# Kernel optimization log

Measured on AMD Instinct MI355X. Metric: run time of the kernel, lower is better.

## Reference

```python
import jax, jax.numpy as jnp
import numpy as np

EMBED_DIM = 2048
NUM_HEADS = 16
HEAD_DIM = EMBED_DIM // NUM_HEADS
SCALE = 1.0 / float(np.sqrt(HEAD_DIM))
B, L = 2, 2048


def setup_inputs() -> dict:
    key = jax.random.key(0)
    ks = jax.random.split(key, 8)
    s_in = 1.0 / np.sqrt(EMBED_DIM)
    return {
        "query": jax.random.normal(ks[0], (B, L, EMBED_DIM), dtype=jnp.float32),
        "key": jax.random.normal(ks[1], (B, L, EMBED_DIM), dtype=jnp.float32),
        "value": jax.random.normal(ks[2], (B, L, EMBED_DIM), dtype=jnp.float32),
        # in_proj: Linear(E, 3E) -> weight [3E, E], bias [3E]
        "W_in": jax.random.uniform(ks[3], (3 * EMBED_DIM, EMBED_DIM), jnp.float32, -s_in, s_in),
        "b_in": jax.random.uniform(ks[4], (3 * EMBED_DIM,), jnp.float32, -s_in, s_in),
        # out_proj: Linear(E, E) -> weight [E, E], bias [E]
        "W_out": jax.random.uniform(ks[5], (EMBED_DIM, EMBED_DIM), jnp.float32, -s_in, s_in),
        "b_out": jax.random.uniform(ks[6], (EMBED_DIM,), jnp.float32, -s_in, s_in),
    }


def reference(query, key, value, W_in, b_in, W_out, b_out):
    # NOTE: the torch module ignores `key`/`value`; QKV all come from `query`.
    b, t, e = query.shape
    qkv = jnp.einsum("ble,fe->blf", query, W_in) + b_in  # [B, L, 3E]
    q, k, v = jnp.split(qkv, 3, axis=-1)
    # [B, H, L, D]
    q = q.reshape(b, t, NUM_HEADS, HEAD_DIM).transpose(0, 2, 1, 3)
    k = k.reshape(b, -1, NUM_HEADS, HEAD_DIM).transpose(0, 2, 1, 3)
    v = v.reshape(b, -1, NUM_HEADS, HEAD_DIM).transpose(0, 2, 1, 3)
    scores = jnp.einsum("bhqd,bhkd->bhqk", q, k) * SCALE  # [B, H, L, L]
    attn = jax.nn.softmax(scores, axis=-1)
    # torch code zeros attn if any NaN appears (can't happen with no masks);
    # replicate the guard harmlessly:
    attn = jnp.where(jnp.any(jnp.isnan(attn)), jnp.zeros_like(attn), attn)
    ctx = jnp.einsum("bhqk,bhkd->bhqd", attn, v)  # [B, H, L, D]
    ctx = ctx.transpose(0, 2, 1, 3).reshape(b, t, e)  # [B, L, E]
    out = jnp.einsum("ble,fe->blf", ctx, W_out) + b_out
    attn_avg = attn.mean(axis=1)  # [B, L, L]
    return (out, attn_avg)
```

## Files before the change

### kernel.cpp

```cpp
#include <hip/hip_runtime.h>
#include <hip/hip_bf16.h>
#include <stdint.h>
#include <stddef.h>

constexpr int BATCH = 2;
constexpr int SEQ   = 2048;
constexpr int EMBD  = 2048;
constexpr int NHEAD = 16;
constexpr int HDIM  = 128;
constexpr float QSCALE = 0.08838834764831845f * 1.4426950408889634f;

typedef short bf16x8 __attribute__((ext_vector_type(8)));
typedef float f32x4  __attribute__((ext_vector_type(4)));

__device__ __forceinline__ short f2bfs(float f) {
  union { __hip_bfloat16 h; short s; } u;
  u.h = __float2bfloat16(f);
  return u.s;
}

__device__ __forceinline__ void gload_lds16(const void* g, void* l) {
  __builtin_amdgcn_global_load_lds(
      (const __attribute__((address_space(1))) unsigned int*)g,
      (__attribute__((address_space(3))) unsigned int*)l, 16, 0, 0);
}

__device__ __forceinline__ int vperm(int k) {
  return (k & ~31) | (k & 3) | (((k >> 4) & 1) << 2) | (((k >> 2) & 3) << 3);
}

__global__ void cvt_bf16(const float* __restrict__ in, unsigned short* __restrict__ out, int n) {
  int i = (blockIdx.x * blockDim.x + threadIdx.x) * 8;
  const int stride = gridDim.x * blockDim.x * 8;
  for (; i + 7 < n; i += stride) {
    float4 a = *(const float4*)(in + i);
    float4 b = *(const float4*)(in + i + 4);
    union { unsigned short u[8]; int4 v; } r;
    r.u[0] = (unsigned short)f2bfs(a.x); r.u[1] = (unsigned short)f2bfs(a.y);
    r.u[2] = (unsigned short)f2bfs(a.z); r.u[3] = (unsigned short)f2bfs(a.w);
    r.u[4] = (unsigned short)f2bfs(b.x); r.u[5] = (unsigned short)f2bfs(b.y);
    r.u[6] = (unsigned short)f2bfs(b.z); r.u[7] = (unsigned short)f2bfs(b.w);
    *(int4*)(out + i) = r.v;
  }
}

struct EpiQKV {
  const float* bias;
  unsigned short* qs; unsigned short* ks; unsigned short* vti;
  __device__ void operator()(int row, int col, float v) const {
    float val = v + bias[col];
    const int which = col >> 11;
    const int h = (col >> 7) & 15;
    const int d = col & 127;
    const int b = row >> 11, l = row & (SEQ - 1);
    if (which == 0) {
      qs[(((unsigned)(b * NHEAD + h) * SEQ) + l) * HDIM + d] = (unsigned short)f2bfs(val * QSCALE);
    } else if (which == 1) {
      ks[(((unsigned)(b * NHEAD + h) * SEQ) + l) * HDIM + d] = (unsigned short)f2bfs(val);
    } else {
      vti[(((unsigned)(b * NHEAD + h) * HDIM) + d) * SEQ + vperm(l)] = (unsigned short)f2bfs(val);
    }
  }
};

struct EpiOut {
  const float* bias;
  float* out;
  __device__ void operator()(int row, int col, float v) const {
    out[(size_t)row * EMBD + col] = v + bias[col];
  }
};

template <class Epi>
__global__ __launch_bounds__(256, 2) void gemm_bt(
    const unsigned short* __restrict__ A, const unsigned short* __restrict__ B,
    int K, Epi epi) {
  __shared__ __align__(16) unsigned short lds[2][8192];
  const int tid = threadIdx.x;
  const int w = tid >> 6, lane = tid & 63;
  const int g = lane >> 4, lr = lane & 15;
  const int wm = w >> 1, wn = w & 1;
  const int m0 = blockIdx.y * 128, n0 = blockIdx.x * 128;
  const int srow = lane >> 2, sslot = lane & 3;

  f32x4 acc[4][4] = {};

  auto stage = [&](int buf, int t) {
    const int k0 = t * 32;
#pragma unroll
    for (int c2 = 0; c2 < 2; ++c2) {
      const int chunk = 2 * w + c2;
      const int row = chunk * 16 + srow;
      const int kel = k0 + ((sslot ^ ((row >> 1) & 3)) << 3);
      gload_lds16(A + (size_t)(m0 + row) * K + kel, &lds[buf][chunk * 512]);
      gload_lds16(B + (size_t)(n0 + row) * K + kel, &lds[buf][4096 + chunk * 512]);
    }
  };

  const int nt = K >> 5;
  int cur = 0;
  stage(0, 0);
  asm volatile("s_waitcnt vmcnt(0)" ::: "memory");
  __syncthreads();

  for (int t = 0; t < nt; ++t) {
    if (t + 1 < nt) stage(cur ^ 1, t + 1);
    bf16x8 af[4], bq[4];
#pragma unroll
    for (int fr = 0; fr < 4; ++fr) {
      const int r = wm * 64 + fr * 16 + lr;
      af[fr] = *(const bf16x8*)&lds[cur][r * 32 + ((g ^ ((r >> 1) & 3)) << 3)];
      const int rn = wn * 64 + fr * 16 + lr;
      bq[fr] = *(const bf16x8*)&lds[cur][4096 + rn * 32 + ((g ^ ((rn >> 1) & 3)) << 3)];
    }
#pragma unroll
    for (int i = 0; i < 4; ++i)
#pragma unroll
      for (int j = 0; j < 4; ++j)
        acc[i][j] = __builtin_amdgcn_mfma_f32_16x16x32_bf16(af[i], bq[j], acc[i][j], 0, 0, 0);
    asm volatile("s_waitcnt vmcnt(0)" ::: "memory");
    __syncthreads();
    cur ^= 1;
  }

#pragma unroll
  for (int i = 0; i < 4; ++i)
#pragma unroll
    for (int j = 0; j < 4; ++j) {
      const int row = m0 + wm * 64 + i * 16 + g * 4;
      const int col = n0 + wn * 64 + j * 16 + lr;
#pragma unroll
      for (int jr = 0; jr < 4; ++jr) epi(row + jr, col, acc[i][j][jr]);
    }
}

__global__ __launch_bounds__(256, 2) void flash_fwd(
    const unsigned short* __restrict__ qs, const unsigned short* __restrict__ ks,
    const unsigned short* __restrict__ vti, unsigned short* __restrict__ ctx,
    float* __restrict__ c_s) {
  __shared__ __align__(16) unsigned short smem[2][16384];
  const int tid = threadIdx.x, w = tid >> 6, lane = tid & 63;
  const int g = lane >> 4, lr = lane & 15;
  const int blk = blockIdx.x;
  const int qt = blk & 31, h = (blk >> 5) & 15, b = blk >> 9;
  const int q0 = qt * 64;
  const size_t bh = ((size_t)(b * NHEAD + h)) * SEQ * HDIM;

  const int qrow = q0 + w * 16 + lr;
  bf16x8 qf[4];
#pragma unroll
  for (int kk = 0; kk < 4; ++kk)
    qf[kk] = *(const bf16x8*)(qs + bh + (size_t)qrow * HDIM + kk * 32 + g * 8);

  float m_run = -1e30f, l_run = 0.f;
  f32x4 o[8] = {};

  auto stage = [&](int buf, int t) {
    unsigned short* kt = smem[buf];
    unsigned short* vt = smem[buf] + 8192;
    const int key0 = t * 64;
#pragma unroll
    for (int c = 0; c < 4; ++c) {
      const int chunk = w * 4 + c;
      const int key = chunk * 4 + (lane >> 4);
      const int slot = lane & 15;
      gload_lds16(ks + bh + (size_t)(key0 + key) * HDIM + ((slot ^ (key & 7)) * 8),
                  &kt[chunk * 512]);
    }
#pragma unroll
    for (int c = 0; c < 4; ++c) {
      const int chunk = w * 4 + c;
      const int d = chunk * 8 + (lane >> 3);
      const int slot = lane & 7;
      gload_lds16(vti + bh + (size_t)d * SEQ + key0 + ((slot ^ (d & 7)) * 8),
                  &vt[chunk * 512]);
    }
  };

  stage(0, 0);
  asm volatile("s_waitcnt vmcnt(0)" ::: "memory");
  __syncthreads();
  int cur = 0;

  for (int t = 0; t < 32; ++t) {
    if (t + 1 < 32) stage(cur ^ 1, t + 1);
    const unsigned short* kt = smem[cur];
    const unsigned short* vt = smem[cur] + 8192;

    f32x4 st[4] = {};
#pragma unroll
    for (int kk = 0; kk < 4; ++kk)
#pragma unroll
      for (int fc = 0; fc < 4; ++fc) {
        const int key = fc * 16 + lr;
        bf16x8 kf = *(const bf16x8*)&kt[key * 128 + (((kk * 4 + g) ^ (key & 7)) << 3)];
        st[fc] = __builtin_amdgcn_mfma_f32_16x16x32_bf16(kf, qf[kk], st[fc], 0, 0, 0);
      }

    float tmax = st[0][0];
#pragma unroll
    for (int fc = 0; fc < 4; ++fc)
#pragma unroll
      for (int j = 0; j < 4; ++j) tmax = fmaxf(tmax, st[fc][j]);
    tmax = fmaxf(tmax, __shfl_xor(tmax, 16));
    tmax = fmaxf(tmax, __shfl_xor(tmax, 32));
    if (!__all(tmax <= m_run + 8.f)) {
      const float m_new = fmaxf(m_run, tmax);
      const float corr = __builtin_exp2f(m_run - m_new);
      l_run *= corr;
#pragma unroll
      for (int fd = 0; fd < 8; ++fd)
#pragma unroll
        for (int j = 0; j < 4; ++j) o[fd][j] *= corr;
      m_run = m_new;
    }
    float pt[4][4];
    float tsum = 0.f;
#pragma unroll
    for (int fc = 0; fc < 4; ++fc)
#pragma unroll
      for (int j = 0; j < 4; ++j) {
        const float e = __builtin_exp2f(st[fc][j] - m_run);
        pt[fc][j] = e; tsum += e;
      }
    tsum += __shfl_xor(tsum, 16);
    tsum += __shfl_xor(tsum, 32);
    l_run += tsum;

    bf16x8 pb[2];
#pragma unroll
    for (int c = 0; c < 2; ++c)
#pragma unroll
      for (int j = 0; j < 4; ++j) {
        pb[c][j]     = f2bfs(pt[2 * c][j]);
        pb[c][4 + j] = f2bfs(pt[2 * c + 1][j]);
      }

#pragma unroll
    for (int fd = 0; fd < 8; ++fd) {
      const int d = fd * 16 + lr;
#pragma unroll
      for (int c = 0; c < 2; ++c) {
        bf16x8 vf = *(const bf16x8*)&vt[d * 64 + (((c * 4 + g) ^ (d & 7)) << 3)];
        o[fd] = __builtin_amdgcn_mfma_f32_16x16x32_bf16(vf, pb[c], o[fd], 0, 0, 0);
      }
    }

    asm volatile("s_waitcnt vmcnt(0)" ::: "memory");
    __syncthreads();
    cur ^= 1;
  }

  const float inv_l = 1.0f / l_run;
  unsigned short* trp = smem[0] + w * 2176;
#pragma unroll
  for (int fd = 0; fd < 8; ++fd)
#pragma unroll
    for (int jp = 0; jp < 2; ++jp) {
      const int d = fd * 16 + 4 * g + 2 * jp;
      unsigned valu = (unsigned)(unsigned short)f2bfs(o[fd][2 * jp] * inv_l) |
                      ((unsigned)(unsigned short)f2bfs(o[fd][2 * jp + 1] * inv_l) << 16);
      *(unsigned*)((char*)trp + lr * 272 + d * 2) = valu;
    }
  __syncthreads();
#pragma unroll
  for (int r4 = 0; r4 < 4; ++r4) {
    const int row = r4 * 4 + g;
    bf16x8 valv = *(const bf16x8*)((char*)trp + row * 272 + lr * 16);
    *(bf16x8*)(ctx + (size_t)(b * SEQ + q0 + w * 16 + row) * EMBD + h * HDIM + lr * 8) = valv;
  }
  if (g == 0) {
    const int ridx = (b * NHEAD + h) * SEQ + q0 + w * 16 + lr;
    c_s[ridx] = m_run + __log2f(l_run) + 4.0f;
  }
}

__global__ __launch_bounds__(256, 2) void attn_avg_k(
    const unsigned short* __restrict__ qs, const unsigned short* __restrict__ ks,
    const float* __restrict__ c_s, float* __restrict__ out) {
  __shared__ __align__(16) unsigned short lds[32768];
  unsigned short* qlds = lds;
  unsigned short* klds = lds + 16384;
  const int tid = threadIdx.x, w = tid >> 6, lane = tid & 63;
  const int g = lane >> 4, lr = lane & 15;
  const int wm = w >> 1, wn = w & 1;
  const int blk = blockIdx.x;
  const int k0 = (blk & 15) * 128, q0 = ((blk >> 4) & 15) * 128, b = blk >> 8;

  const int srow = lane >> 4, sslot = lane & 15;

  f32x4 acc[4][4] = {};

  for (int h = 0; h < NHEAD; ++h) {
    const size_t bh = ((size_t)(b * NHEAD + h)) * SEQ * HDIM;
    if (h) __syncthreads();
#pragma unroll
    for (int c = 0; c < 8; ++c) {
      const int chunk = w * 8 + c;
      const int row = chunk * 4 + srow;
      const int kel = (sslot ^ (row & 15)) * 8;
      gload_lds16(qs + bh + (size_t)(q0 + row) * HDIM + kel, &qlds[chunk * 512]);
      gload_lds16(ks + bh + (size_t)(k0 + row) * HDIM + kel, &klds[chunk * 512]);
    }
    asm volatile("s_waitcnt vmcnt(0)" ::: "memory");
    __syncthreads();

    f32x4 st[4][4] = {};
#pragma unroll
    for (int kk = 0; kk < 4; ++kk) {
      bf16x8 af[4], bq[4];
#pragma unroll
      for (int fr = 0; fr < 4; ++fr) {
        const int rq = wm * 64 + fr * 16 + lr;
        af[fr] = *(const bf16x8*)&qlds[rq * 128 + (((kk * 4 + g) ^ (rq & 15)) << 3)];
        const int rk = wn * 64 + fr * 16 + lr;
        bq[fr] = *(const bf16x8*)&klds[rk * 128 + (((kk * 4 + g) ^ (rk & 15)) << 3)];
      }
#pragma unroll
      for (int i = 0; i < 4; ++i)
#pragma unroll
        for (int j = 0; j < 4; ++j)
          st[i][j] = __builtin_amdgcn_mfma_f32_16x16x32_bf16(af[i], bq[j], st[i][j], 0, 0, 0);
    }

    const int chq = (b * NHEAD + h) * SEQ + q0 + wm * 64 + g * 4;
#pragma unroll
    for (int i = 0; i < 4; ++i) {
      const f32x4 cq = *(const f32x4*)&c_s[chq + i * 16];
#pragma unroll
      for (int j = 0; j < 4; ++j)
#pragma unroll
        for (int jr = 0; jr < 4; ++jr)
          acc[i][j][jr] += __builtin_exp2f(st[i][j][jr] - cq[jr]);
    }
  }

#pragma unroll
  for (int i = 0; i < 4; ++i)
#pragma unroll
    for (int jr = 0; jr < 4; ++jr) {
      const size_t rowoff = (size_t)(b * SEQ + q0 + wm * 64 + i * 16 + g * 4 + jr) * SEQ;
#pragma unroll
      for (int j = 0; j < 4; ++j)
        out[rowoff + k0 + wn * 64 + j * 16 + lr] = acc[i][j][jr];
    }
}

extern "C" void kernel_launch(void* const* d_in, const int* in_sizes, int n_in,
                              void* d_out, int out_size, void* d_ws, size_t ws_size,
                              hipStream_t stream) {
  const float* query = (const float*)d_in[0];
  const float* W_in  = (const float*)d_in[3];
  const float* b_in  = (const float*)d_in[4];
  const float* W_out = (const float*)d_in[5];
  const float* b_out = (const float*)d_in[6];

  float* out      = (float*)d_out;
  float* attn_avg = out + (size_t)BATCH * SEQ * EMBD;

  char* ws = (char*)d_ws;
  auto take = [&](size_t bytes) { char* p = ws; ws += bytes; return p; };
  const size_t szBLE = (size_t)BATCH * SEQ * EMBD * 2;
  unsigned short* qbf = (unsigned short*)take(szBLE);
  unsigned short* wi  = (unsigned short*)take((size_t)3 * EMBD * EMBD * 2);
  unsigned short* wo  = (unsigned short*)take((size_t)EMBD * EMBD * 2);
  unsigned short* qsb = (unsigned short*)take(szBLE);
  unsigned short* ksb = (unsigned short*)take(szBLE);
  unsigned short* vti = (unsigned short*)take(szBLE);
  unsigned short* ctx = (unsigned short*)take(szBLE);
  float* c_s = (float*)take((size_t)BATCH * NHEAD * SEQ * 4);

  cvt_bf16<<<1024, 256, 0, stream>>>(query, qbf, BATCH * SEQ * EMBD);
  cvt_bf16<<<2048, 256, 0, stream>>>(W_in, wi, 3 * EMBD * EMBD);
  cvt_bf16<<<1024, 256, 0, stream>>>(W_out, wo, EMBD * EMBD);

  gemm_bt<EpiQKV><<<dim3(48, 32), 256, 0, stream>>>(qbf, wi, EMBD,
                                                    EpiQKV{b_in, qsb, ksb, vti});
  flash_fwd<<<BATCH * NHEAD * (SEQ / 64), 256, 0, stream>>>(qsb, ksb, vti, ctx, c_s);
  gemm_bt<EpiOut><<<dim3(16, 32), 256, 0, stream>>>(ctx, wo, EMBD, EpiOut{b_out, out});
  attn_avg_k<<<BATCH * (SEQ / 128) * (SEQ / 128), 256, 0, stream>>>(qsb, ksb, c_s, attn_avg);
}
```

Before: 411.4 us.

## Use 256x256-tile 8-wave pipelined GEMM for QKV projection

Adds a new GEMM kernel with 256x256 output tiles, 512 threads and a 64-wide K step, used for the QKV input projection. It splits each K step into four quadrant phases that interleave LDS reads, next-tile global-to-LDS loads and MFMA bursts under s_setprio. It also remaps block IDs across 8 groups, likely to match the XCD layout and improve L2 reuse. The larger tile cuts global and LDS traffic per FLOP, at the cost of more registers and 128KB of LDS per block. The fixed-count vmcnt waits and the barrier-heavy schedule are fragile if any load count changes.

```diff
diff --git a/kernel.cpp b/kernel.cpp
--- a/kernel.cpp
+++ b/kernel.cpp
@@ -72,6 +72,135 @@
 };
 
 template <class Epi>
+__global__ __launch_bounds__(512, 2) void gemm_bt8(
+    const unsigned short* __restrict__ A, const unsigned short* __restrict__ B,
+    const int K, const int NBX, Epi epi) {
+  __shared__ __align__(16) unsigned short lds[2][32768];
+  const int tid = threadIdx.x, w = tid >> 6, lane = tid & 63;
+  const int g = lane >> 4, lr = lane & 15;
+  const int wm = w >> 2, wn = w & 3;
+
+  const int cpx = gridDim.x >> 3;
+  const int bid = ((int)blockIdx.x & 7) * cpx + ((int)blockIdx.x >> 3);
+  const int m0 = (bid / NBX) * 256, n0 = (bid % NBX) * 256;
+
+  const int nt = K >> 6;
+  const int srow = tid >> 3, sslot = tid & 7;
+
+  auto stageA = [&](int t, int hh) {
+    const int kel = t * 64 + ((sslot ^ (srow & 7)) << 3);
+#pragma unroll
+    for (int l = 0; l < 2; ++l)
+      gload_lds16(A + (size_t)(m0 + hh * 128 + l * 64 + srow) * K + kel,
+                  &lds[t & 1][hh * 8192 + l * 4096 + w * 512]);
+  };
+  auto stageB = [&](int t, int hh) {
+    const int kel = t * 64 + ((sslot ^ (srow & 7)) << 3);
+#pragma unroll
+    for (int l = 0; l < 2; ++l)
+      gload_lds16(B + (size_t)(n0 + hh * 128 + l * 64 + srow) * K + kel,
+                  &lds[t & 1][16384 + hh * 8192 + l * 4096 + w * 512]);
+  };
+  auto rdA = [&](int buf, int Mh, int kk, int fr) -> bf16x8 {
+    const int row = wm * 128 + Mh * 64 + fr * 16 + lr;
+    return *(const bf16x8*)&lds[buf][row * 64 + (((kk * 4 + g) ^ (row & 7)) << 3)];
+  };
+  auto rdB = [&](int buf, int Nh, int kk, int fb) -> bf16x8 {
+    const int row = wn * 64 + Nh * 32 + fb * 16 + lr;
+    return *(const bf16x8*)&lds[buf][16384 + row * 64 + (((kk * 4 + g) ^ (row & 7)) << 3)];
+  };
+
+  f32x4 acc[8][4] = {};
+  bf16x8 a[4][2], bn0[2][2], bn1[2][2];
+
+  stageA(0, 0); stageA(0, 1); stageB(0, 0); stageB(0, 1);
+  if (nt > 1) { stageA(1, 0);
+    asm volatile("s_waitcnt vmcnt(2)" ::: "memory");
+  } else {
+    asm volatile("s_waitcnt vmcnt(0)" ::: "memory");
+  }
+  __builtin_amdgcn_s_barrier();
+
+  for (int t = 0; t < nt; ++t) {
+    const int buf = t & 1;
+#pragma unroll
+    for (int fr = 0; fr < 4; ++fr) { a[fr][0] = rdA(buf, 0, 0, fr); a[fr][1] = rdA(buf, 0, 1, fr); }
+#pragma unroll
+    for (int fb = 0; fb < 2; ++fb) { bn0[fb][0] = rdB(buf, 0, 0, fb); bn0[fb][1] = rdB(buf, 0, 1, fb); }
+    if (t + 1 < nt) stageA(t + 1, 1);
+    __builtin_amdgcn_s_barrier();
+    asm volatile("s_waitcnt lgkmcnt(0)" ::: "memory");
+    __builtin_amdgcn_s_setprio(1);
+#pragma unroll
+    for (int fr = 0; fr < 4; ++fr)
+#pragma unroll
+      for (int fb = 0; fb < 2; ++fb)
+#pragma unroll
+        for (int kk = 0; kk < 2; ++kk)
+          acc[fr][fb] = __builtin_amdgcn_mfma_f32_16x16x32_bf16(a[fr][kk], bn0[fb][kk], acc[fr][fb], 0, 0, 0);
+    __builtin_amdgcn_s_setprio(0);
+    __builtin_amdgcn_s_barrier();
+#pragma unroll
+    for (int fb = 0; fb < 2; ++fb) { bn1[fb][0] = rdB(buf, 1, 0, fb); bn1[fb][1] = rdB(buf, 1, 1, fb); }
+    if (t + 1 < nt) stageB(t + 1, 0);
+    __builtin_amdgcn_s_barrier();
+    asm volatile("s_waitcnt lgkmcnt(0)" ::: "memory");
+    __builtin_amdgcn_s_setprio(1);
+#pragma unroll
+    for (int fr = 0; fr < 4; ++fr)
+#pragma unroll
+      for (int fb = 0; fb < 2; ++fb)
+#pragma unroll
+        for (int kk = 0; kk < 2; ++kk)
+          acc[fr][2 + fb] = __builtin_amdgcn_mfma_f32_16x16x32_bf16(a[fr][kk], bn1[fb][kk], acc[fr][2 + fb], 0, 0, 0);
+    __builtin_amdgcn_s_setprio(0);
+    __builtin_amdgcn_s_barrier();
+#pragma unroll
+    for (int fr = 0; fr < 4; ++fr) { a[fr][0] = rdA(buf, 1, 0, fr); a[fr][1] = rdA(buf, 1, 1, fr); }
+    if (t + 1 < nt) stageB(t + 1, 1);
+    __builtin_amdgcn_s_barrier();
+    asm volatile("s_waitcnt lgkmcnt(0)" ::: "memory");
+    __builtin_amdgcn_s_setprio(1);
+#pragma unroll
+    for (int fr = 0; fr < 4; ++fr)
+#pragma unroll
+      for (int fb = 0; fb < 2; ++fb)
+#pragma unroll
+        for (int kk = 0; kk < 2; ++kk)
+          acc[4 + fr][2 + fb] = __builtin_amdgcn_mfma_f32_16x16x32_bf16(a[fr][kk], bn1[fb][kk], acc[4 + fr][2 + fb], 0, 0, 0);
+    __builtin_amdgcn_s_setprio(0);
+    __builtin_amdgcn_s_barrier();
+    if (t + 2 < nt) stageA(t + 2, 0);
+    __builtin_amdgcn_s_barrier();
+    __builtin_amdgcn_s_setprio(1);
+#pragma unroll
+    for (int fr = 0; fr < 4; ++fr)
+#pragma unroll
+      for (int fb = 0; fb < 2; ++fb)
+#pragma unroll
+        for (int kk = 0; kk < 2; ++kk)
+          acc[4 + fr][fb] = __builtin_amdgcn_mfma_f32_16x16x32_bf16(a[fr][kk], bn0[fb][kk], acc[4 + fr][fb], 0, 0, 0);
+    __builtin_amdgcn_s_setprio(0);
+    if (t + 2 < nt) {
+      asm volatile("s_waitcnt vmcnt(2)" ::: "memory");
+    } else if (t + 1 < nt) {
+      asm volatile("s_waitcnt vmcnt(0)" ::: "memory");
+    }
+    __builtin_amdgcn_s_barrier();
+  }
+
+#pragma unroll
+  for (int mf = 0; mf < 8; ++mf)
+#pragma unroll
+    for (int nf = 0; nf < 4; ++nf) {
+      const int row = m0 + wm * 128 + mf * 16 + g * 4;
+      const int col = n0 + wn * 64 + nf * 16 + lr;
+#pragma unroll
+      for (int jr = 0; jr < 4; ++jr) epi(row + jr, col, acc[mf][nf][jr]);
+    }
+}
+
+template <class Epi>
 __global__ __launch_bounds__(256, 2) void gemm_bt(
     const unsigned short* __restrict__ A, const unsigned short* __restrict__ B,
     int K, Epi epi) {
@@ -374,8 +503,8 @@
   cvt_bf16<<<2048, 256, 0, stream>>>(W_in, wi, 3 * EMBD * EMBD);
   cvt_bf16<<<1024, 256, 0, stream>>>(W_out, wo, EMBD * EMBD);
 
-  gemm_bt<EpiQKV><<<dim3(48, 32), 256, 0, stream>>>(qbf, wi, EMBD,
-                                                    EpiQKV{b_in, qsb, ksb, vti});
+  gemm_bt8<EpiQKV><<<384, 512, 0, stream>>>(qbf, wi, EMBD, 24,
+                                            EpiQKV{b_in, qsb, ksb, vti});
   flash_fwd<<<BATCH * NHEAD * (SEQ / 64), 256, 0, stream>>>(qsb, ksb, vti, ctx, c_s);
   gemm_bt<EpiOut><<<dim3(16, 32), 256, 0, stream>>>(ctx, wo, EMBD, EpiOut{b_out, out});
   attn_avg_k<<<BATCH * (SEQ / 128) * (SEQ / 128), 256, 0, stream>>>(qsb, ksb, c_s, attn_avg);
```

Result: no change. 419.3 us (+1.9%).

## Triple-buffer Q/K staging in attn_avg kernel with per-32-dim chunk pipelining

Applied to the files above, without the earlier changes.

Replaces the per-head load-all-then-compute scheme in the attention-average kernel with a 3-slot ring buffer of 32-dim chunks of Q and K, prefetching two chunks ahead. Waits now use vmcnt(4) plus raw s_barrier instead of a full drain each head, so global loads can overlap MFMA work. LDS use drops from 64KB to 48KB per block, and the swizzle changes to match 32-element rows. The price is more barriers per head and some risk of subtle ring-buffer synchronisation mistakes.

```diff
diff --git a/kernel.cpp b/kernel.cpp
--- a/kernel.cpp
+++ b/kernel.cpp
@@ -278,52 +278,64 @@
 __global__ __launch_bounds__(256, 2) void attn_avg_k(
     const unsigned short* __restrict__ qs, const unsigned short* __restrict__ ks,
     const float* __restrict__ c_s, float* __restrict__ out) {
-  __shared__ __align__(16) unsigned short lds[32768];
-  unsigned short* qlds = lds;
-  unsigned short* klds = lds + 16384;
+  __shared__ __align__(16) unsigned short lds[3][8192];
   const int tid = threadIdx.x, w = tid >> 6, lane = tid & 63;
   const int g = lane >> 4, lr = lane & 15;
   const int wm = w >> 1, wn = w & 1;
   const int blk = blockIdx.x;
   const int k0 = (blk & 15) * 128, q0 = ((blk >> 4) & 15) * 128, b = blk >> 8;
-
-  const int srow = lane >> 4, sslot = lane & 15;
+  const int srow = lane >> 2, sslot = lane & 3;
+
+  constexpr int NC = NHEAD * 4;
+
+  auto stage = [&](int c) {
+    const size_t bh = ((size_t)(b * NHEAD + (c >> 2))) * SEQ * HDIM + (c & 3) * 32;
+    unsigned short* slot = lds[c % 3];
+#pragma unroll
+    for (int c2 = 0; c2 < 2; ++c2) {
+      const int chunk = 2 * w + c2;
+      const int row = chunk * 16 + srow;
+      const int kel = (sslot ^ ((row >> 1) & 3)) << 3;
+      gload_lds16(qs + bh + (size_t)(q0 + row) * HDIM + kel, &slot[chunk * 512]);
+      gload_lds16(ks + bh + (size_t)(k0 + row) * HDIM + kel, &slot[4096 + chunk * 512]);
+    }
+  };
 
   f32x4 acc[4][4] = {};
 
-  for (int h = 0; h < NHEAD; ++h) {
-    const size_t bh = ((size_t)(b * NHEAD + h)) * SEQ * HDIM;
-    if (h) __syncthreads();
-#pragma unroll
-    for (int c = 0; c < 8; ++c) {
-      const int chunk = w * 8 + c;
-      const int row = chunk * 4 + srow;
-      const int kel = (sslot ^ (row & 15)) * 8;
-      gload_lds16(qs + bh + (size_t)(q0 + row) * HDIM + kel, &qlds[chunk * 512]);
-      gload_lds16(ks + bh + (size_t)(k0 + row) * HDIM + kel, &klds[chunk * 512]);
-    }
-    asm volatile("s_waitcnt vmcnt(0)" ::: "memory");
-    __syncthreads();
-
+  stage(0); stage(1);
+  asm volatile("s_waitcnt vmcnt(4)" ::: "memory");
+  asm volatile("s_barrier" ::: "memory");
+
+  for (int hc = 0; hc < NHEAD; ++hc) {
     f32x4 st[4][4] = {};
 #pragma unroll
-    for (int kk = 0; kk < 4; ++kk) {
+    for (int dq = 0; dq < 4; ++dq) {
+      const int c = hc * 4 + dq;
+      if (c + 2 < NC) stage(c + 2);
+      const unsigned short* slot = lds[c % 3];
       bf16x8 af[4], bq[4];
 #pragma unroll
       for (int fr = 0; fr < 4; ++fr) {
         const int rq = wm * 64 + fr * 16 + lr;
-        af[fr] = *(const bf16x8*)&qlds[rq * 128 + (((kk * 4 + g) ^ (rq & 15)) << 3)];
+        af[fr] = *(const bf16x8*)&slot[rq * 32 + ((g ^ ((rq >> 1) & 3)) << 3)];
         const int rk = wn * 64 + fr * 16 + lr;
-        bq[fr] = *(const bf16x8*)&klds[rk * 128 + (((kk * 4 + g) ^ (rk & 15)) << 3)];
+        bq[fr] = *(const bf16x8*)&slot[4096 + rk * 32 + ((g ^ ((rk >> 1) & 3)) << 3)];
       }
 #pragma unroll
       for (int i = 0; i < 4; ++i)
 #pragma unroll
         for (int j = 0; j < 4; ++j)
           st[i][j] = __builtin_amdgcn_mfma_f32_16x16x32_bf16(af[i], bq[j], st[i][j], 0, 0, 0);
-    }
-
-    const int chq = (b * NHEAD + h) * SEQ + q0 + wm * 64 + g * 4;
+      if (c + 2 < NC) {
+        asm volatile("s_waitcnt vmcnt(4)" ::: "memory");
+        asm volatile("s_barrier" ::: "memory");
+      } else if (c + 1 < NC) {
+        asm volatile("s_waitcnt vmcnt(0)" ::: "memory");
+        asm volatile("s_barrier" ::: "memory");
+      }
+    }
+    const int chq = (b * NHEAD + hc) * SEQ + q0 + wm * 64 + g * 4;
 #pragma unroll
     for (int i = 0; i < 4; ++i) {
       const f32x4 cq = *(const f32x4*)&c_s[chq + i * 16];
```

Result: faster. 399.0 us (-3.0%).
